# Performance work log

Hardware: AMD Instinct MI355X
Metric: run time of the kernel (lower is better)

## Reference

```python
import jax, jax.numpy as jnp
import numpy as np

N = 208   # number of nodes (hard-coded ring graph in source)
K = 4     # k-hop receptive field

def _support(n=N, k=K):
    # ring adjacency: node i connected to i-1 and i+1 (wrap-around)
    A = np.zeros((n, n), dtype=np.float64)
    idx = np.arange(n)
    A[idx, (idx + 1) % n] = 1.0
    A[idx, (idx - 1) % n] = 1.0
    # normalized_laplacian in source: adj + diag(1/deg)
    L = A + np.diag(1.0 / A.sum(axis=1))
    # calculate_adjacency_k: sign(L^k) -> band mask of width 2k+1
    Lk = np.linalg.matrix_power(L, k)
    return np.sign(Lk).astype(np.float32)


def setup_inputs() -> dict:
    key = jax.random.key(0)
    k1, k2 = jax.random.split(key)
    B, T = 64, 2048
    x = jax.random.normal(k1, (B, T, N), dtype=jnp.float32)
    # per-node non-shared kernel [N, N], glorot-ish scale
    W = jax.random.normal(k2, (N, N), dtype=jnp.float32) * (1.0 / np.sqrt(N))
    b = jnp.zeros((N,), dtype=jnp.float32)
    S = jnp.asarray(_support())  # fixed k-hop adjacency mask
    return {"x": x, "W": W, "b": b, "S": S}


def reference(x, W, b, S):
    # Locally-connected GC: mask the [N,N] kernel by the k-hop support,
    # then apply as a node-mixing linear transform per (batch, time).
    out = jnp.einsum('btn,nm->btm', x, S * W) + b
    return out  # activation=None in init
```

## Files before the change

kernel.cpp:

```cpp
#include <hip/hip_runtime.h>


#define NN   208
#define NC   52
#define HW   4
#define BAND 9
#define TR   16
#define THREADS 832
#define NBLK 512
#define TILE_F  (TR * NN)
#define TILE_F4 (TILE_F / 4)

typedef float vfloat4 __attribute__((ext_vector_type(4)));

__global__ __launch_bounds__(THREADS) void lcgc_kernel(
    const float* __restrict__ x,
    const float* __restrict__ W,
    const float* __restrict__ b,
    const float* __restrict__ S,
    float* __restrict__ out,
    int total_rows)
{
    __shared__ float sX[2][TILE_F];
    __shared__ float sBand[BAND * NN];

    const int tid = threadIdx.x;

    for (int i = tid; i < BAND * NN; i += THREADS) {
        int d = i / NN;
        int m = i - d * NN;
        int n = m + d - HW;
        if (n < 0) n += NN;
        else if (n >= NN) n -= NN;
        sBand[i] = W[n * NN + m] * S[n * NN + m];
    }
    __syncthreads();

    const int c    = tid % NC;
    const int rg   = tid / NC;
    const int wave = tid >> 6;

    const float4 bias4 = *reinterpret_cast<const float4*>(&b[c * 4]);
    const int cm = (c == 0)      ? NC - 1 : c - 1;
    const int cp = (c == NC - 1) ? 0      : c + 1;

    const long long ntiles_total = total_rows / TR;
    const long long nt = ntiles_total / gridDim.x;
    const long long t0 = (long long)blockIdx.x * nt;

    float* const ldst0 = &sX[0][wave * 256];
    float* const ldst1 = &sX[1][wave * 256];

    #define STAGE(kt, bi)                                                     \
        do {                                                                  \
            const float* gsrc = x + (t0 + (kt)) * TILE_F + (long long)tid * 4;\
            __builtin_amdgcn_global_load_lds(                                 \
                (const __attribute__((address_space(1))) void*)(gsrc),        \
                (__attribute__((address_space(3))) void*)((bi) ? ldst1 : ldst0),\
                16, 0, 0);                                                    \
        } while (0)

    #define COMPUTE(kt, bi)                                                   \
        do {                                                                  \
            const float4* xr4 =                                               \
                reinterpret_cast<const float4*>(&sX[(bi)][rg * NN]);          \
            const float4 a = xr4[cm];                                         \
            const float4 m4 = xr4[c];                                         \
            const float4 e = xr4[cp];                                         \
            const float xv[12] = {a.x, a.y, a.z, a.w,                         \
                                  m4.x, m4.y, m4.z, m4.w,                     \
                                  e.x, e.y, e.z, e.w};                        \
            float4 acc = bias4;                                               \
            const float4* band4 = reinterpret_cast<const float4*>(sBand);     \
            _Pragma("unroll")                                                 \
            for (int d = 0; d < BAND; ++d) {                                  \
                const float4 bd = band4[d * NC + c];                          \
                acc.x = fmaf(bd.x, xv[0 + d], acc.x);                         \
                acc.y = fmaf(bd.y, xv[1 + d], acc.y);                         \
                acc.z = fmaf(bd.z, xv[2 + d], acc.z);                         \
                acc.w = fmaf(bd.w, xv[3 + d], acc.w);                         \
            }                                                                 \
            vfloat4 av = {acc.x, acc.y, acc.z, acc.w};                        \
            __builtin_nontemporal_store(av, reinterpret_cast<vfloat4*>(       \
                out + (t0 + (kt)) * TILE_F + rg * NN + c * 4));               \
        } while (0)

    STAGE(0, 0);

    for (long long k = 0; k < nt - 1; ++k) {
        STAGE(k + 1, (int)((k + 1) & 1));
        asm volatile("s_waitcnt vmcnt(1)" ::: "memory");
        __builtin_amdgcn_sched_barrier(0);
        __builtin_amdgcn_s_barrier();
        COMPUTE(k, (int)(k & 1));
        asm volatile("" ::: "memory");
        __builtin_amdgcn_s_barrier();
    }
    asm volatile("s_waitcnt vmcnt(0)" ::: "memory");
    __builtin_amdgcn_sched_barrier(0);
    __builtin_amdgcn_s_barrier();
    COMPUTE(nt - 1, (int)((nt - 1) & 1));

    #undef STAGE
    #undef COMPUTE
}

extern "C" void kernel_launch(void* const* d_in, const int* in_sizes, int n_in,
                              void* d_out, int out_size, void* d_ws, size_t ws_size,
                              hipStream_t stream) {
    const float* x = (const float*)d_in[0];
    const float* W = (const float*)d_in[1];
    const float* b = (const float*)d_in[2];
    const float* S = (const float*)d_in[3];
    float* out = (float*)d_out;

    const int total_rows = in_sizes[0] / NN;
    lcgc_kernel<<<dim3(NBLK), dim3(THREADS), 0, stream>>>(
        x, W, b, S, out, total_rows);
}
```

Baseline: 43.27 us.

## Deepen LDS prefetch pipeline from double to four-stage buffering

Replaces the two-slot LDS ring with four slots, prefetching three tiles ahead via global_load_lds. The vmcnt wait count accounts for the async loads and the nontemporal stores still outstanding, so each tile's load has completed before compute. More loads in flight per block are meant to hide HBM latency in this bandwidth-bound kernel. LDS use grows to about 60KB per block, which may limit occupancy, and the wait-count bookkeeping is fragile.

```diff
diff --git a/kernel.cpp b/kernel.cpp
--- a/kernel.cpp
+++ b/kernel.cpp
@@ -9,7 +9,7 @@
 #define THREADS 832
 #define NBLK 512
 #define TILE_F  (TR * NN)
-#define TILE_F4 (TILE_F / 4)
+#define DEPTH 4
 
 typedef float vfloat4 __attribute__((ext_vector_type(4)));
 
@@ -21,7 +21,7 @@
     float* __restrict__ out,
     int total_rows)
 {
-    __shared__ float sX[2][TILE_F];
+    __shared__ float sX[DEPTH][TILE_F];
     __shared__ float sBand[BAND * NN];
 
     const int tid = threadIdx.x;
@@ -48,22 +48,22 @@
     const long long nt = ntiles_total / gridDim.x;
     const long long t0 = (long long)blockIdx.x * nt;
 
-    float* const ldst0 = &sX[0][wave * 256];
-    float* const ldst1 = &sX[1][wave * 256];
+    float* const ldsw = &sX[0][wave * 256];
 
-    #define STAGE(kt, bi)                                                     \
+    #define STAGE(kt)                                                         \
         do {                                                                  \
             const float* gsrc = x + (t0 + (kt)) * TILE_F + (long long)tid * 4;\
+            float* ldst = ldsw + (int)((kt) & (DEPTH - 1)) * TILE_F;          \
             __builtin_amdgcn_global_load_lds(                                 \
                 (const __attribute__((address_space(1))) void*)(gsrc),        \
-                (__attribute__((address_space(3))) void*)((bi) ? ldst1 : ldst0),\
+                (__attribute__((address_space(3))) void*)(ldst),              \
                 16, 0, 0);                                                    \
         } while (0)
 
-    #define COMPUTE(kt, bi)                                                   \
+    #define COMPUTE(kt)                                                       \
         do {                                                                  \
-            const float4* xr4 =                                               \
-                reinterpret_cast<const float4*>(&sX[(bi)][rg * NN]);          \
+            const float4* xr4 = reinterpret_cast<const float4*>(              \
+                &sX[(int)((kt) & (DEPTH - 1))][rg * NN]);                     \
             const float4 a = xr4[cm];                                         \
             const float4 m4 = xr4[c];                                         \
             const float4 e = xr4[cp];                                         \
@@ -85,21 +85,29 @@
                 out + (t0 + (kt)) * TILE_F + rg * NN + c * 4));               \
         } while (0)
 
-    STAGE(0, 0);
+    STAGE(0); STAGE(1); STAGE(2);
 
-    for (long long k = 0; k < nt - 1; ++k) {
-        STAGE(k + 1, (int)((k + 1) & 1));
-        asm volatile("s_waitcnt vmcnt(1)" ::: "memory");
+    for (long long k = 0; k < nt; ++k) {
+        if (k + 3 < nt) STAGE(k + 3);
+        {
+            const int a1 = (int)(k < 3 ? k : 3);
+            const int a2 = (int)((nt - 1 - k) < 3 ? (nt - 1 - k) : 3);
+            switch (a1 + a2) {
+            case 0: asm volatile("s_waitcnt vmcnt(0)" ::: "memory"); break;
+            case 1: asm volatile("s_waitcnt vmcnt(1)" ::: "memory"); break;
+            case 2: asm volatile("s_waitcnt vmcnt(2)" ::: "memory"); break;
+            case 3: asm volatile("s_waitcnt vmcnt(3)" ::: "memory"); break;
+            case 4: asm volatile("s_waitcnt vmcnt(4)" ::: "memory"); break;
+            case 5: asm volatile("s_waitcnt vmcnt(5)" ::: "memory"); break;
+            default: asm volatile("s_waitcnt vmcnt(6)" ::: "memory"); break;
+            }
+        }
         __builtin_amdgcn_sched_barrier(0);
         __builtin_amdgcn_s_barrier();
-        COMPUTE(k, (int)(k & 1));
+        COMPUTE(k);
         asm volatile("" ::: "memory");
         __builtin_amdgcn_s_barrier();
     }
-    asm volatile("s_waitcnt vmcnt(0)" ::: "memory");
-    __builtin_amdgcn_sched_barrier(0);
-    __builtin_amdgcn_s_barrier();
-    COMPUTE(nt - 1, (int)((nt - 1) & 1));
 
     #undef STAGE
     #undef COMPUTE
```

Measured after the change: 51.66 us. 19.4% more time.
